# Performance work log

Hardware: AMD Instinct MI355X
Metric: run time of the kernel (lower is better)

## Reference

```python
import jax, jax.numpy as jnp
import numpy as np

EMBED_DIM = 1024
SEQ = 1024  # must equal EMBED_DIM due to the module's mask construction
BATCH = 8


def setup_inputs() -> dict:
    key = jax.random.key(0)
    ks = jax.random.split(key, 7)
    s = 1.0 / np.sqrt(EMBED_DIM)
    return {
        "x": jax.random.normal(ks[0], (BATCH, SEQ, EMBED_DIM), jnp.float32),
        "Wq": jax.random.normal(ks[1], (EMBED_DIM, EMBED_DIM), jnp.float32) * s,
        "bq": jax.random.normal(ks[2], (EMBED_DIM,), jnp.float32) * s,
        "Wk": jax.random.normal(ks[3], (EMBED_DIM, EMBED_DIM), jnp.float32) * s,
        "bk": jax.random.normal(ks[4], (EMBED_DIM,), jnp.float32) * s,
        "Wv": jax.random.normal(ks[5], (EMBED_DIM, EMBED_DIM), jnp.float32) * s,
        "bv": jax.random.normal(ks[6], (EMBED_DIM,), jnp.float32) * s,
    }


def reference(x, Wq, bq, Wk, bk, Wv, bv):
    # nn.Linear: y = x @ W.T + b
    q = jnp.einsum("bse,oe->bso", x, Wq) + bq
    k = jnp.einsum("bse,oe->bso", x, Wk) + bk
    v = jnp.einsum("bse,oe->bso", x, Wv) + bv
    scores = jnp.einsum("bqd,bkd->bqk", q, k) / jnp.sqrt(jnp.float32(EMBED_DIM))
    # causal mask: tril(ones(E, E)) applied to [B, S, S] scores (S == E)
    causal = jnp.tril(jnp.ones((SEQ, SEQ), dtype=bool))
    scores = jnp.where(causal, scores, jnp.float32(-1e9))
    attn = jax.nn.softmax(scores, axis=-1)
    return jnp.einsum("bqk,bkd->bqd", attn, v)
```

## Files before the change

### kernel.cpp

```cpp
#include <hip/hip_runtime.h>
#include <hip/hip_bf16.h>

typedef unsigned short u16;
typedef __bf16 bf16x8 __attribute__((ext_vector_type(8)));
typedef float f32x4 __attribute__((ext_vector_type(4)));

#define AS1 __attribute__((address_space(1)))
#define AS3 __attribute__((address_space(3)))

__device__ inline void gload_lds16(const void* g, void* l) {
    __builtin_amdgcn_global_load_lds((const AS1 void*)g, (AS3 void*)l, 16, 0, 0);
}

__device__ inline u16 f2bf(float f) {
    __hip_bfloat16 h = __float2bfloat16(f);
    return __builtin_bit_cast(u16, h);
}

__global__ __launch_bounds__(256)
void cvt_all(const float4* __restrict__ x,  const float4* __restrict__ wq,
             const float4* __restrict__ wk, const float4* __restrict__ wv,
             u16* __restrict__ xb, u16* __restrict__ Wb) {
    int i = blockIdx.x * 256 + threadIdx.x;
    const float4* src; u16* dst; int off;
    if (i < 2097152)      { src = x;  dst = xb;            off = i; }
    else if (i < 2359296) { src = wq; dst = Wb;            off = i - 2097152; }
    else if (i < 2621440) { src = wk; dst = Wb + 1048576;  off = i - 2359296; }
    else                  { src = wv; dst = Wb + 2097152;  off = i - 2621440; }
    float4 v = src[off];
    uint2 pk;
    pk.x = (unsigned)f2bf(v.x) | ((unsigned)f2bf(v.y) << 16);
    pk.y = (unsigned)f2bf(v.z) | ((unsigned)f2bf(v.w) << 16);
    *(uint2*)(dst + (long long)off * 4) = pk;
}

__global__ __launch_bounds__(256)
void transpose_v(const u16* __restrict__ V, u16* __restrict__ Vt) {
    __shared__ u16 tile[32][33];
    const int b  = blockIdx.z;
    const int d0 = blockIdx.x * 32;
    const int k0 = blockIdx.y * 32;
    const int tx = threadIdx.x & 31;
    const int ty = threadIdx.x >> 5;
    #pragma unroll
    for (int r = ty; r < 32; r += 8)
        tile[r][tx] = V[((long long)b * 1024 + k0 + r) * 1024 + d0 + tx];
    __syncthreads();
    #pragma unroll
    for (int r = ty; r < 32; r += 8)
        Vt[((long long)b * 1024 + d0 + r) * 1024 + k0 + tx] = tile[tx][r];
}

template<int MODE>
__global__ __launch_bounds__(256)
void gemm_bt(const u16* __restrict__ A, long long strideA,
             const u16* __restrict__ Bt, long long strideB,
             void* __restrict__ Cv, long long strideC,
             const float* __restrict__ bias0, const float* __restrict__ bias1,
             const float* __restrict__ bias2,
             int N, int K, float scale)
{
    constexpr int BK = 64;
    __shared__ __align__(16) u16 shA[128 * BK];
    __shared__ __align__(16) u16 shB[128 * BK];
    int bz, row0, col0;
    if (MODE == 0) {
        bz   = blockIdx.z;
        row0 = (blockIdx.x * 8 + (blockIdx.y & 7)) * 128;
        col0 = (int)(blockIdx.y >> 3) * 128;
    } else {
        bz   = blockIdx.x;
        row0 = blockIdx.y * 128;
        col0 = blockIdx.z * 128;
    }
    if (MODE == 1 && col0 > row0) return;
    const u16* Ab = A  + (long long)bz * strideA + (long long)row0 * K;
    const u16* Bb = Bt + (long long)bz * strideB + (long long)col0 * K;
    int kEnd = K;
    if (MODE == 2) kEnd = (row0 + 128 < K) ? (row0 + 128) : K;

    const int t  = (int)threadIdx.x;
    const int l  = t & 63;
    const int w  = t >> 6;
    const int wr = w >> 1, wc = w & 1;
    const int fr = l & 15, fq = l >> 4;

    f32x4 acc[4][4];
    #pragma unroll
    for (int m = 0; m < 4; ++m)
        #pragma unroll
        for (int n = 0; n < 4; ++n)
            acc[m][n] = (f32x4){0.f, 0.f, 0.f, 0.f};

    int aOff[2][4], bOff[2][4];
    #pragma unroll
    for (int kh = 0; kh < 2; ++kh) {
        const int g = ((kh * 4 + fq) ^ (fr & 7)) * 8;
        #pragma unroll
        for (int m = 0; m < 4; ++m) aOff[kh][m] = (wr * 64 + m * 16 + fr) * 64 + g;
        #pragma unroll
        for (int n = 0; n < 4; ++n) bOff[kh][n] = (wc * 64 + n * 16 + fr) * 64 + g;
    }

    for (int kk = 0; kk < kEnd; kk += BK) {
        if (kk) __syncthreads();
        #pragma unroll
        for (int r = 0; r < 4; ++r) {
            const int s  = t + r * 256;
            const int rw = s >> 3;
            const int g  = (s & 7) ^ (rw & 7);
            gload_lds16(Ab + (long long)rw * K + kk + g * 8, (void*)(shA + s * 8));
            gload_lds16(Bb + (long long)rw * K + kk + g * 8, (void*)(shB + s * 8));
        }
        __syncthreads();
        bf16x8 aF[2][4], bF[2][4];
        #pragma unroll
        for (int kh = 0; kh < 2; ++kh) {
            #pragma unroll
            for (int m = 0; m < 4; ++m) aF[kh][m] = *(const bf16x8*)(shA + aOff[kh][m]);
            #pragma unroll
            for (int n = 0; n < 4; ++n) bF[kh][n] = *(const bf16x8*)(shB + bOff[kh][n]);
        }
        #pragma unroll
        for (int kh = 0; kh < 2; ++kh)
            #pragma unroll
            for (int m = 0; m < 4; ++m)
                #pragma unroll
                for (int n = 0; n < 4; ++n)
                    acc[m][n] = __builtin_amdgcn_mfma_f32_16x16x32_bf16(aF[kh][m], bF[kh][n], acc[m][n], 0, 0, 0);
    }

    if (MODE == 0) {
        const float* bp = (bz == 0) ? bias0 : ((bz == 1) ? bias1 : bias2);
        u16* C = (u16*)Cv + (long long)bz * strideC;
        #pragma unroll
        for (int n = 0; n < 4; ++n) {
            const int cn = col0 + wc * 64 + n * 16 + fr;
            const float bv = bp[cn];
            #pragma unroll
            for (int m = 0; m < 4; ++m) {
                const int cm = row0 + wr * 64 + m * 16 + fq * 4;
                #pragma unroll
                for (int j = 0; j < 4; ++j)
                    C[(long long)(cm + j) * N + cn] = f2bf(acc[m][n][j] + bv);
            }
        }
    } else {
        float* C = (float*)Cv + (long long)bz * strideC;
        #pragma unroll
        for (int n = 0; n < 4; ++n) {
            const int cn = col0 + wc * 64 + n * 16 + fr;
            #pragma unroll
            for (int m = 0; m < 4; ++m) {
                const int cm = row0 + wr * 64 + m * 16 + fq * 4;
                #pragma unroll
                for (int j = 0; j < 4; ++j)
                    C[(long long)(cm + j) * N + cn] = acc[m][n][j] * scale;
            }
        }
    }
}

__global__ __launch_bounds__(256)
void softmax_causal(const float* __restrict__ S, u16* __restrict__ P) {
    __shared__ float redM[4], redS[4];
    const int row = blockIdx.x;
    const int q   = row & 1023;
    const int t   = (int)threadIdx.x;
    const int l   = t & 63, w = t >> 6;
    const int j0  = t * 4;
    float x0 = -1e30f, x1 = -1e30f, x2 = -1e30f, x3 = -1e30f;
    if (j0 <= q) {
        float4 v = ((const float4*)(S + (long long)row * 1024))[t];
        x0 = v.x;
        x1 = (j0 + 1 <= q) ? v.y : -1e30f;
        x2 = (j0 + 2 <= q) ? v.z : -1e30f;
        x3 = (j0 + 3 <= q) ? v.w : -1e30f;
    }
    float m = fmaxf(fmaxf(x0, x1), fmaxf(x2, x3));
    #pragma unroll
    for (int o = 32; o > 0; o >>= 1) m = fmaxf(m, __shfl_xor(m, o, 64));
    if (l == 0) redM[w] = m;
    __syncthreads();
    m = fmaxf(fmaxf(redM[0], redM[1]), fmaxf(redM[2], redM[3]));
    float e0 = __expf(x0 - m);
    float e1 = __expf(x1 - m);
    float e2 = __expf(x2 - m);
    float e3 = __expf(x3 - m);
    float s = e0 + e1 + e2 + e3;
    #pragma unroll
    for (int o = 32; o > 0; o >>= 1) s += __shfl_xor(s, o, 64);
    if (l == 0) redS[w] = s;
    __syncthreads();
    s = redS[0] + redS[1] + redS[2] + redS[3];
    const float inv = 1.0f / s;
    uint2 pk;
    pk.x = (unsigned)f2bf(e0 * inv) | ((unsigned)f2bf(e1 * inv) << 16);
    pk.y = (unsigned)f2bf(e2 * inv) | ((unsigned)f2bf(e3 * inv) << 16);
    *(uint2*)(P + (long long)row * 1024 + j0) = pk;
}

extern "C" void kernel_launch(void* const* d_in, const int* in_sizes, int n_in,
                              void* d_out, int out_size, void* d_ws, size_t ws_size,
                              hipStream_t stream) {
    const float* x  = (const float*)d_in[0];
    const float* Wq = (const float*)d_in[1];
    const float* bq = (const float*)d_in[2];
    const float* Wk = (const float*)d_in[3];
    const float* bk = (const float*)d_in[4];
    const float* Wv = (const float*)d_in[5];
    const float* bv = (const float*)d_in[6];
    float* out = (float*)d_out;
    char* ws = (char*)d_ws;

    u16*   xb  = (u16*)(ws + 0);
    u16*   Wb  = (u16*)(ws + ((size_t)16 << 20));
    u16*   QKV = (u16*)(ws + ((size_t)22 << 20));
    u16*   Vt  = (u16*)(ws + ((size_t)70 << 20));
    float* SC  = (float*)(ws + ((size_t)86 << 20));
    u16*   P   = (u16*)(ws + ((size_t)118 << 20));

    cvt_all<<<11264, 256, 0, stream>>>((const float4*)x, (const float4*)Wq,
                                       (const float4*)Wk, (const float4*)Wv, xb, Wb);

    gemm_bt<0><<<dim3(8, 64, 3), 256, 0, stream>>>(xb, 0LL, Wb, 1048576LL, QKV, 8388608LL,
                                                   bq, bk, bv, 1024, 1024, 1.0f);

    transpose_v<<<dim3(32, 32, 8), 256, 0, stream>>>(QKV + 2 * 8388608LL, Vt);

    gemm_bt<1><<<dim3(8, 8, 8), 256, 0, stream>>>(QKV, 1048576LL, QKV + 8388608LL, 1048576LL,
                                                  SC, 1048576LL, nullptr, nullptr, nullptr,
                                                  1024, 1024, 0.03125f);

    softmax_causal<<<8192, 256, 0, stream>>>(SC, P);

    gemm_bt<2><<<dim3(8, 8, 8), 256, 0, stream>>>(P, 1048576LL, Vt, 1048576LL, out, 1048576LL,
                                                  nullptr, nullptr, nullptr,
                                                  1024, 1024, 1.0f);
}
```

Measured before the change: 124.8 us.

## Compute V transposed directly via swapped GEMM, store scores in bf16

The separate V transpose kernel is removed. V^T is now produced directly by a new GEMM mode that multiplies Wv by x, giving a [1024, 8192] layout, and the PV GEMM reads it with a row stride. The score matrix is written as bf16 instead of fp32, which halves score write and read traffic in the softmax. The PV GEMM also launches diagonal row tiles in reverse order so the heaviest causal tiles start first. Rounding scores to bf16 before softmax adds precision error.

```diff
diff --git a/kernel.cpp b/kernel.cpp
--- a/kernel.cpp
+++ b/kernel.cpp
@@ -15,6 +15,9 @@
 __device__ inline u16 f2bf(float f) {
     __hip_bfloat16 h = __float2bfloat16(f);
     return __builtin_bit_cast(u16, h);
+}
+__device__ inline float bf2f(unsigned u) {
+    return __builtin_bit_cast(float, u << 16);
 }
 
 __global__ __launch_bounds__(256)
@@ -34,31 +37,13 @@
     *(uint2*)(dst + (long long)off * 4) = pk;
 }
 
-__global__ __launch_bounds__(256)
-void transpose_v(const u16* __restrict__ V, u16* __restrict__ Vt) {
-    __shared__ u16 tile[32][33];
-    const int b  = blockIdx.z;
-    const int d0 = blockIdx.x * 32;
-    const int k0 = blockIdx.y * 32;
-    const int tx = threadIdx.x & 31;
-    const int ty = threadIdx.x >> 5;
-    #pragma unroll
-    for (int r = ty; r < 32; r += 8)
-        tile[r][tx] = V[((long long)b * 1024 + k0 + r) * 1024 + d0 + tx];
-    __syncthreads();
-    #pragma unroll
-    for (int r = ty; r < 32; r += 8)
-        Vt[((long long)b * 1024 + d0 + r) * 1024 + k0 + tx] = tile[tx][r];
-}
-
 template<int MODE>
 __global__ __launch_bounds__(256)
-void gemm_bt(const u16* __restrict__ A, long long strideA,
-             const u16* __restrict__ Bt, long long strideB,
-             void* __restrict__ Cv, long long strideC,
+void gemm_bt(const u16* __restrict__ A, long long strideAb,
+             const u16* __restrict__ Bt, long long strideBb,
+             void* __restrict__ Cv, long long strideCb,
              const float* __restrict__ bias0, const float* __restrict__ bias1,
-             const float* __restrict__ bias2,
-             int N, int K, float scale)
+             int N, int K, int strideBrow, float scale)
 {
     constexpr int BK = 64;
     __shared__ __align__(16) u16 shA[128 * BK];
@@ -68,16 +53,24 @@
         bz   = blockIdx.z;
         row0 = (blockIdx.x * 8 + (blockIdx.y & 7)) * 128;
         col0 = (int)(blockIdx.y >> 3) * 128;
-    } else {
+    } else if (MODE == 3) {
+        bz   = 0;
+        col0 = (blockIdx.x * 8 + (blockIdx.y & 7)) * 128;
+        row0 = (int)(blockIdx.y >> 3) * 128;
+    } else if (MODE == 1) {
         bz   = blockIdx.x;
         row0 = blockIdx.y * 128;
         col0 = blockIdx.z * 128;
+    } else {
+        bz   = blockIdx.x;
+        row0 = (7 - (int)blockIdx.y) * 128;
+        col0 = blockIdx.z * 128;
     }
     if (MODE == 1 && col0 > row0) return;
-    const u16* Ab = A  + (long long)bz * strideA + (long long)row0 * K;
-    const u16* Bb = Bt + (long long)bz * strideB + (long long)col0 * K;
+    const u16* Ab = A  + bz * strideAb + (long long)row0 * K;
+    const u16* Bb = Bt + bz * strideBb + (long long)col0 * strideBrow;
     int kEnd = K;
-    if (MODE == 2) kEnd = (row0 + 128 < K) ? (row0 + 128) : K;
+    if (MODE == 2) kEnd = row0 + 128;
 
     const int t  = (int)threadIdx.x;
     const int l  = t & 63;
@@ -110,7 +103,7 @@
             const int rw = s >> 3;
             const int g  = (s & 7) ^ (rw & 7);
             gload_lds16(Ab + (long long)rw * K + kk + g * 8, (void*)(shA + s * 8));
-            gload_lds16(Bb + (long long)rw * K + kk + g * 8, (void*)(shB + s * 8));
+            gload_lds16(Bb + (long long)rw * strideBrow + kk + g * 8, (void*)(shB + s * 8));
         }
         __syncthreads();
         bf16x8 aF[2][4], bF[2][4];
@@ -131,8 +124,8 @@
     }
 
     if (MODE == 0) {
-        const float* bp = (bz == 0) ? bias0 : ((bz == 1) ? bias1 : bias2);
-        u16* C = (u16*)Cv + (long long)bz * strideC;
+        const float* bp = (bz == 0) ? bias0 : bias1;
+        u16* C = (u16*)Cv + bz * strideCb;
         #pragma unroll
         for (int n = 0; n < 4; ++n) {
             const int cn = col0 + wc * 64 + n * 16 + fr;
@@ -145,24 +138,50 @@
                     C[(long long)(cm + j) * N + cn] = f2bf(acc[m][n][j] + bv);
             }
         }
+    } else if (MODE == 3) {
+        u16* C = (u16*)Cv;
+        #pragma unroll
+        for (int n = 0; n < 4; ++n) {
+            const int cn = col0 + wc * 64 + n * 16 + fr;
+            #pragma unroll
+            for (int m = 0; m < 4; ++m) {
+                const int cm = row0 + wr * 64 + m * 16 + fq * 4;
+                #pragma unroll
+                for (int j = 0; j < 4; ++j)
+                    C[(long long)(cm + j) * N + cn] = f2bf(acc[m][n][j] + bias0[cm + j]);
+            }
+        }
+    } else if (MODE == 1) {
+        u16* C = (u16*)Cv + bz * strideCb;
+        #pragma unroll
+        for (int n = 0; n < 4; ++n) {
+            const int cn = col0 + wc * 64 + n * 16 + fr;
+            #pragma unroll
+            for (int m = 0; m < 4; ++m) {
+                const int cm = row0 + wr * 64 + m * 16 + fq * 4;
+                #pragma unroll
+                for (int j = 0; j < 4; ++j)
+                    C[(long long)(cm + j) * N + cn] = f2bf(acc[m][n][j] * scale);
+            }
+        }
     } else {
-        float* C = (float*)Cv + (long long)bz * strideC;
-        #pragma unroll
-        for (int n = 0; n < 4; ++n) {
-            const int cn = col0 + wc * 64 + n * 16 + fr;
-            #pragma unroll
-            for (int m = 0; m < 4; ++m) {
-                const int cm = row0 + wr * 64 + m * 16 + fq * 4;
-                #pragma unroll
-                for (int j = 0; j < 4; ++j)
-                    C[(long long)(cm + j) * N + cn] = acc[m][n][j] * scale;
+        float* C = (float*)Cv + bz * strideCb;
+        #pragma unroll
+        for (int n = 0; n < 4; ++n) {
+            const int cn = col0 + wc * 64 + n * 16 + fr;
+            #pragma unroll
+            for (int m = 0; m < 4; ++m) {
+                const int cm = row0 + wr * 64 + m * 16 + fq * 4;
+                #pragma unroll
+                for (int j = 0; j < 4; ++j)
+                    C[(long long)(cm + j) * N + cn] = acc[m][n][j];
             }
         }
     }
 }
 
 __global__ __launch_bounds__(256)
-void softmax_causal(const float* __restrict__ S, u16* __restrict__ P) {
+void softmax_causal(const u16* __restrict__ S, u16* __restrict__ P) {
     __shared__ float redM[4], redS[4];
     const int row = blockIdx.x;
     const int q   = row & 1023;
@@ -171,11 +190,11 @@
     const int j0  = t * 4;
     float x0 = -1e30f, x1 = -1e30f, x2 = -1e30f, x3 = -1e30f;
     if (j0 <= q) {
-        float4 v = ((const float4*)(S + (long long)row * 1024))[t];
-        x0 = v.x;
-        x1 = (j0 + 1 <= q) ? v.y : -1e30f;
-        x2 = (j0 + 2 <= q) ? v.z : -1e30f;
-        x3 = (j0 + 3 <= q) ? v.w : -1e30f;
+        uint2 raw = *(const uint2*)(S + (long long)row * 1024 + j0);
+        x0 = bf2f(raw.x & 0xffffu);
+        x1 = (j0 + 1 <= q) ? bf2f(raw.x >> 16) : -1e30f;
+        x2 = (j0 + 2 <= q) ? bf2f(raw.y & 0xffffu) : -1e30f;
+        x3 = (j0 + 3 <= q) ? bf2f(raw.y >> 16) : -1e30f;
     }
     float m = fmaxf(fmaxf(x0, x1), fmaxf(x2, x3));
     #pragma unroll
@@ -213,28 +232,29 @@
     float* out = (float*)d_out;
     char* ws = (char*)d_ws;
 
-    u16*   xb  = (u16*)(ws + 0);
-    u16*   Wb  = (u16*)(ws + ((size_t)16 << 20));
-    u16*   QKV = (u16*)(ws + ((size_t)22 << 20));
-    u16*   Vt  = (u16*)(ws + ((size_t)70 << 20));
-    float* SC  = (float*)(ws + ((size_t)86 << 20));
-    u16*   P   = (u16*)(ws + ((size_t)118 << 20));
+    u16* xb  = (u16*)(ws + 0);
+    u16* Wb  = (u16*)(ws + ((size_t)16 << 20));
+    u16* QK  = (u16*)(ws + ((size_t)22 << 20));
+    u16* Vt  = (u16*)(ws + ((size_t)54 << 20));
+    u16* SC  = (u16*)(ws + ((size_t)70 << 20));
+    u16* P   = (u16*)(ws + ((size_t)86 << 20));
 
     cvt_all<<<11264, 256, 0, stream>>>((const float4*)x, (const float4*)Wq,
                                        (const float4*)Wk, (const float4*)Wv, xb, Wb);
 
-    gemm_bt<0><<<dim3(8, 64, 3), 256, 0, stream>>>(xb, 0LL, Wb, 1048576LL, QKV, 8388608LL,
-                                                   bq, bk, bv, 1024, 1024, 1.0f);
-
-    transpose_v<<<dim3(32, 32, 8), 256, 0, stream>>>(QKV + 2 * 8388608LL, Vt);
-
-    gemm_bt<1><<<dim3(8, 8, 8), 256, 0, stream>>>(QKV, 1048576LL, QKV + 8388608LL, 1048576LL,
-                                                  SC, 1048576LL, nullptr, nullptr, nullptr,
-                                                  1024, 1024, 0.03125f);
+    gemm_bt<0><<<dim3(8, 64, 2), 256, 0, stream>>>(xb, 0LL, Wb, 1048576LL, QK, 8388608LL,
+                                                   bq, bk, 1024, 1024, 1024, 1.0f);
+
+    gemm_bt<3><<<dim3(8, 64), 256, 0, stream>>>(Wb + 2097152, 0LL, xb, 0LL, Vt, 0LL,
+                                                bv, nullptr, 8192, 1024, 1024, 1.0f);
+
+    gemm_bt<1><<<dim3(8, 8, 8), 256, 0, stream>>>(QK, 1048576LL, QK + 8388608LL, 1048576LL,
+                                                  SC, 1048576LL, nullptr, nullptr,
+                                                  1024, 1024, 1024, 0.03125f);
 
     softmax_causal<<<8192, 256, 0, stream>>>(SC, P);
 
-    gemm_bt<2><<<dim3(8, 8, 8), 256, 0, stream>>>(P, 1048576LL, Vt, 1048576LL, out, 1048576LL,
-                                                  nullptr, nullptr, nullptr,
-                                                  1024, 1024, 1.0f);
-}
+    gemm_bt<2><<<dim3(8, 8, 8), 256, 0, stream>>>(P, 1048576LL, Vt, 1024LL, out, 1048576LL,
+                                                  nullptr, nullptr,
+                                                  1024, 1024, 8192, 1.0f);
+}
```

New measurement: 125.4 us. Within noise of the previous version (+0.5%).
